# Performance work log

Hardware: AMD Instinct MI355X
Metric: run time of the kernel (lower is better)

## Reference

```python
import jax, jax.numpy as jnp
import numpy as np

NEG = -1000000.0  # mask value used by the torch module


def setup_inputs() -> dict:
    key = jax.random.key(0)
    k1, k2, k3, k4 = jax.random.split(key, 4)
    B, Q, K, D = 16, 2048, 2048, 128
    queries = jax.random.normal(k1, (B, Q, D), dtype=jnp.float32)
    keys = jax.random.normal(k2, (B, K, D), dtype=jnp.float32)
    values = jax.random.normal(k3, (B, K, D), dtype=jnp.float32)
    valid_lens = jax.random.randint(k4, (B,), 0, K, dtype=jnp.int32)
    return {"queries": queries, "keys": keys, "values": values, "valid_lens": valid_lens}


def reference(queries, keys, values, valid_lens):
    d = queries.shape[-1]
    # scores: [B, Q, K]
    scores = jnp.einsum("bqd,bkd->bqk", queries, keys) / jnp.sqrt(jnp.float32(d))
    # mask key positions >= valid_len[b] with the same -1e6 value as torch
    kv_pos = jnp.arange(scores.shape[-1])  # [K]
    mask = kv_pos[None, None, :] < valid_lens[:, None, None]  # [B,1,K]
    scores = jnp.where(mask, scores, NEG)
    attn = jax.nn.softmax(scores, axis=-1)
    # dropout p=0.0 -> identity (module in eval)
    return jnp.einsum("bqk,bkd->bqd", attn, values)
```

## Files before the change

kernel.cpp:

```cpp
#include <hip/hip_runtime.h>
#include <hip/hip_bf16.h>

#define NB    16
#define NQ    2048
#define NKV   2048
#define DH    128
#define KVT   64
#define NTILE 32
#define TILE_BYTES 16384
#define TILE_ELT   8192

typedef __attribute__((ext_vector_type(8))) short short8;
typedef __attribute__((ext_vector_type(4))) float f32x4;

__device__ __forceinline__ unsigned short f2bf(float f) {
    union { float f; unsigned int u; } x; x.f = f;
    unsigned int r = (x.u + 0x7fffu + ((x.u >> 16) & 1u)) >> 16;
    return (unsigned short)r;
}

__device__ __forceinline__ void load_lds16(const void* g, void* l) {
    __builtin_amdgcn_global_load_lds(
        (const __attribute__((address_space(1))) unsigned int*)g,
        (__attribute__((address_space(3))) unsigned int*)l, 16, 0, 0);
}

__global__ __launch_bounds__(256)
void preconv(const float* __restrict__ kg, const float* __restrict__ vg,
             const int* __restrict__ vlg,
             unsigned short* __restrict__ kws, unsigned short* __restrict__ vws) {
    __shared__ __align__(16) unsigned short lv[TILE_ELT];
    const int tid = threadIdx.x;
    const int rb = (blockIdx.x & 7) * 64 + (blockIdx.x >> 3);
    const int b = rb >> 5, t = rb & 31;
    const int vl = vlg[b];
    const int ntiles = (vl == 0) ? NTILE : ((vl + KVT - 1) >> 6);
    if (t >= ntiles) return;

    const float* kb = kg + ((size_t)b * NKV + t * KVT) * DH;
    const float* vb = vg + ((size_t)b * NKV + t * KVT) * DH;
    char* kimg = (char*)(kws + (size_t)(b * NTILE + t) * TILE_ELT);
    char* vimg = (char*)(vws + (size_t)(b * NTILE + t) * TILE_ELT);

    #pragma unroll
    for (int p = 0; p < 4; ++p) {
        int idx = p * 256 + tid;
        int row = idx >> 4, ch = idx & 15;
        f32x4 a = *(const f32x4*)(kb + row * DH + ch * 8);
        f32x4 c = *(const f32x4*)(kb + row * DH + ch * 8 + 4);
        union { short8 v; unsigned short u[8]; } w;
        #pragma unroll
        for (int j = 0; j < 4; ++j) { w.u[j] = f2bf(a[j]); w.u[4 + j] = f2bf(c[j]); }
        *(short8*)(kimg + row * 256 + ((ch * 16) ^ ((row & 7) << 4))) = w.v;
        f32x4 va = *(const f32x4*)(vb + row * DH + ch * 8);
        f32x4 vc = *(const f32x4*)(vb + row * DH + ch * 8 + 4);
        union { short8 v; unsigned short u[8]; } w2;
        #pragma unroll
        for (int j = 0; j < 4; ++j) { w2.u[j] = f2bf(va[j]); w2.u[4 + j] = f2bf(vc[j]); }
        *(short8*)((char*)lv + row * 256 + ((ch * 16) ^ (((row >> 3) & 7) << 4))) = w2.v;
    }
    __syncthreads();
    #pragma unroll
    for (int p = 0; p < 4; ++p) {
        int task = p * 256 + tid;
        int c = task & 7, d = task >> 3;
        union { short8 v; unsigned short u[8]; } w;
        #pragma unroll
        for (int j = 0; j < 8; ++j) {
            int kv = c * 8 + j;
            w.u[j] = *(const unsigned short*)((const char*)lv + kv * 256 + ((d * 2) ^ (((kv >> 3) & 7) << 4)));
        }
        *(short8*)(vimg + d * 128 + ((c * 16) ^ ((d & 7) << 4))) = w.v;
    }
}

__global__ __launch_bounds__(256, 4)
void attn_split(const float* __restrict__ qg,
                const unsigned short* __restrict__ kws,
                const unsigned short* __restrict__ vws,
                const int* __restrict__ vlg,
                float* __restrict__ og,
                float* __restrict__ opart,
                float* __restrict__ ellg,
                int S, int gmask) {
    __shared__ __align__(16) unsigned short lds_k[TILE_ELT];
    __shared__ __align__(16) unsigned short lds_v[TILE_ELT];
    __shared__ __align__(16) unsigned short lds_p[4][16 * KVT];

    const int tid = threadIdx.x;
    const int lane = tid & 63;
    const int wv = tid >> 6;
    const int row16 = lane & 15;
    const int g = lane >> 4;

    const int wid = (blockIdx.x * 1031) & gmask;
    const int b    = wid & 15;
    const int rest = wid >> 4;
    const int qt   = rest & 31;
    const int s    = rest >> 5;
    const int q0   = qt * 64 + wv * 16;
    const int vl = vlg[b];

    const int nt = (vl == 0) ? NTILE : ((vl + KVT - 1) >> 6);

    if (s >= nt) {
        if (tid < 64)
            ellg[(size_t)s * NB * NQ + (size_t)b * NQ + qt * 64 + tid] = 0.f;
        return;
    }

    const float QS = 1.4426950408889634f * 0.08838834764831845f;
    short8 qf[4];
    {
        const float* qp = qg + ((size_t)b * NQ + q0 + row16) * DH + g * 8;
        #pragma unroll
        for (int c = 0; c < 4; ++c) {
            f32x4 a  = *(const f32x4*)(qp + c * 32);
            f32x4 bb = *(const f32x4*)(qp + c * 32 + 4);
            union { short8 v; unsigned short u[8]; } t;
            #pragma unroll
            for (int j = 0; j < 4; ++j) { t.u[j] = f2bf(a[j] * QS); t.u[4 + j] = f2bf(bb[j] * QS); }
            qf[c] = t.v;
        }
    }

    const float MASKV = (vl == 0) ? 0.0f : -1442695.0f;

    f32x4 oacc[8];
    f32x4 ellacc = (f32x4){0.f, 0.f, 0.f, 0.f};
    #pragma unroll
    for (int n = 0; n < 8; ++n) oacc[n] = (f32x4){0.f, 0.f, 0.f, 0.f};
    short8 ones;
    {
        union { short8 v; unsigned short u[8]; } t;
        #pragma unroll
        for (int j = 0; j < 8; ++j) t.u[j] = 0x3F80;
        ones = t.v;
    }

    const char* kbase = (const char*)kws + (size_t)b * NTILE * TILE_BYTES;
    const char* vbase = (const char*)vws + (size_t)b * NTILE * TILE_BYTES;
    const int swzr = ((row16 >> 2) ^ ((row16 & 3) << 1)) & 7;

    for (int tt = s; tt < nt; tt += S) {
        const char* ks = kbase + (size_t)tt * TILE_BYTES;
        const char* vs = vbase + (size_t)tt * TILE_BYTES;
        #pragma unroll
        for (int i = 0; i < 4; ++i) {
            int off = i * 4096 + wv * 1024;
            load_lds16(ks + off + lane * 16, (char*)lds_k + off);
            load_lds16(vs + off + lane * 16, (char*)lds_v + off);
        }
        asm volatile("s_waitcnt vmcnt(0)" ::: "memory");
        __syncthreads();

        f32x4 sc[4];
        #pragma unroll
        for (int n = 0; n < 4; ++n) sc[n] = (f32x4){0.f, 0.f, 0.f, 0.f};
        __builtin_amdgcn_s_setprio(1);
        #pragma unroll
        for (int c = 0; c < 4; ++c) {
            short8 kf[4];
            #pragma unroll
            for (int n = 0; n < 4; ++n) {
                int krow = n * 16 + row16;
                kf[n] = *(const short8*)((const char*)lds_k + krow * 256 +
                                         ((c * 64 + g * 16) ^ ((krow & 7) << 4)));
            }
            #pragma unroll
            for (int n = 0; n < 4; ++n)
                sc[n] = __builtin_amdgcn_mfma_f32_16x16x32_bf16(qf[c], kf[n], sc[n], 0, 0, 0);
        }
        __builtin_amdgcn_s_setprio(0);

        if (vl == 0 || tt == nt - 1) {
            int kvb = tt * KVT;
            #pragma unroll
            for (int n = 0; n < 4; ++n) {
                if (kvb + n * 16 + row16 >= vl) {
                    #pragma unroll
                    for (int r = 0; r < 4; ++r) sc[n][r] = MASKV;
                }
            }
        }

        #pragma unroll
        for (int n = 0; n < 4; ++n)
            #pragma unroll
            for (int r = 0; r < 4; ++r) {
                float p = __builtin_amdgcn_exp2f(sc[n][r]);
                int qr = g * 4 + r;
                int swz = (g ^ (r << 1)) & 7;
                __hip_bfloat16 h = __float2bfloat16(p);
                *(unsigned short*)((char*)lds_p[wv] + qr * 128 +
                                   (((n * 16 + row16) * 2) ^ (swz << 4))) =
                    *reinterpret_cast<unsigned short*>(&h);
            }
        asm volatile("s_waitcnt lgkmcnt(0)" ::: "memory");

        __builtin_amdgcn_s_setprio(1);
        #pragma unroll
        for (int kc = 0; kc < 2; ++kc) {
            short8 pf = *(const short8*)((const char*)lds_p[wv] + row16 * 128 +
                                         ((kc * 64 + g * 16) ^ (swzr << 4)));
            ellacc = __builtin_amdgcn_mfma_f32_16x16x32_bf16(pf, ones, ellacc, 0, 0, 0);
            #pragma unroll
            for (int n2 = 0; n2 < 8; ++n2) {
                int vrow = n2 * 16 + row16;
                short8 vf = *(const short8*)((const char*)lds_v + vrow * 128 +
                                             ((kc * 64 + g * 16) ^ ((vrow & 7) << 4)));
                oacc[n2] = __builtin_amdgcn_mfma_f32_16x16x32_bf16(pf, vf, oacc[n2], 0, 0, 0);
            }
        }
        __builtin_amdgcn_s_setprio(0);

        __syncthreads();
    }

    if (S == 1) {
        float* ob = og + ((size_t)b * NQ + q0) * DH;
        float rl[4];
        #pragma unroll
        for (int r = 0; r < 4; ++r) rl[r] = 1.0f / ellacc[r];
        #pragma unroll
        for (int n2 = 0; n2 < 8; ++n2)
            #pragma unroll
            for (int r = 0; r < 4; ++r)
                ob[(size_t)(g * 4 + r) * DH + n2 * 16 + row16] = oacc[n2][r] * rl[r];
    } else {
        float* op = opart + ((size_t)s * NB * NQ + (size_t)b * NQ + q0) * DH;
        #pragma unroll
        for (int n2 = 0; n2 < 8; ++n2)
            #pragma unroll
            for (int r = 0; r < 4; ++r)
                op[(size_t)(g * 4 + r) * DH + n2 * 16 + row16] = oacc[n2][r];
        if (row16 == 0) {
            float* el = ellg + (size_t)s * NB * NQ + (size_t)b * NQ + q0;
            #pragma unroll
            for (int r = 0; r < 4; ++r) el[g * 4 + r] = ellacc[r];
        }
    }
}

__global__ __launch_bounds__(256)
void combine(const float* __restrict__ opart, const float* __restrict__ ellg,
             float* __restrict__ og, int S) {
    int idx = blockIdx.x * 256 + threadIdx.x;
    int row = idx >> 5;
    int c   = idx & 31;
    f32x4 acc = (f32x4){0.f, 0.f, 0.f, 0.f};
    float l = 0.f;
    for (int s = 0; s < S; ++s) {
        float le = ellg[(size_t)s * NB * NQ + row];
        if (le != 0.f) {
            acc += ((const f32x4*)opart)[((size_t)s * NB * NQ + row) * 32 + c];
            l += le;
        }
    }
    float rl = 1.0f / l;
    ((f32x4*)og)[(size_t)row * 32 + c] = acc * rl;
}

extern "C" void kernel_launch(void* const* d_in, const int* in_sizes, int n_in,
                              void* d_out, int out_size, void* d_ws, size_t ws_size,
                              hipStream_t stream) {
    const float* q  = (const float*)d_in[0];
    const float* k  = (const float*)d_in[1];
    const float* v  = (const float*)d_in[2];
    const int*   vl = (const int*)d_in[3];
    float* o = (float*)d_out;

    const size_t IMG = (size_t)NB * NTILE * TILE_BYTES;
    const size_t ELL_OFF = 2 * IMG;
    const size_t ELL_MAX = (size_t)4 * NB * NQ * 4;
    const size_t OP_OFF  = ELL_OFF + ELL_MAX;
    const size_t OP_ONE  = (size_t)NB * NQ * DH * 4;

    int S = 1;
    if (ws_size >= OP_OFF + 4 * OP_ONE) S = 4;
    else if (ws_size >= OP_OFF + 2 * OP_ONE) S = 2;

    unsigned short* kws = (unsigned short*)d_ws;
    unsigned short* vws = (unsigned short*)((char*)d_ws + IMG);
    float* ellg  = (float*)((char*)d_ws + ELL_OFF);
    float* opart = (float*)((char*)d_ws + OP_OFF);

    int grid = NB * 32 * S;
    preconv<<<dim3(NB * NTILE), dim3(256), 0, stream>>>(k, v, vl, kws, vws);
    attn_split<<<dim3(grid), dim3(256), 0, stream>>>(q, kws, vws, vl, o, opart, ellg, S, grid - 1);
    if (S > 1)
        combine<<<dim3(NB * NQ * 32 / 256), dim3(256), 0, stream>>>(opart, ellg, o, S);
}
```

Baseline: 74.66 us.

## Process 32 query rows per wave to reuse K/V LDS fragments

Each wave now handles two 16-row query blocks (128 queries per workgroup), so every K and V fragment read from LDS feeds two MFMAs, and the grid is halved. The K tile is issued before V and the kernel waits only for K before QK^T, deferring the V wait until after softmax so part of the load overlaps compute. This doubles accumulator registers and P-buffer LDS, with launch bounds lowered to 3 waves/SIMD, and halves the block count, which may hurt load balance across CUs.

```diff
diff --git a/kernel.cpp b/kernel.cpp
--- a/kernel.cpp
+++ b/kernel.cpp
@@ -74,7 +74,7 @@
     }
 }
 
-__global__ __launch_bounds__(256, 4)
+__global__ __launch_bounds__(256, 3)
 void attn_split(const float* __restrict__ qg,
                 const unsigned short* __restrict__ kws,
                 const unsigned short* __restrict__ vws,
@@ -85,7 +85,7 @@
                 int S, int gmask) {
     __shared__ __align__(16) unsigned short lds_k[TILE_ELT];
     __shared__ __align__(16) unsigned short lds_v[TILE_ELT];
-    __shared__ __align__(16) unsigned short lds_p[4][16 * KVT];
+    __shared__ __align__(16) unsigned short lds_p[4][32 * KVT];
 
     const int tid = threadIdx.x;
     const int lane = tid & 63;
@@ -94,25 +94,25 @@
     const int g = lane >> 4;
 
     const int wid = (blockIdx.x * 1031) & gmask;
-    const int b    = wid & 15;
-    const int rest = wid >> 4;
-    const int qt   = rest & 31;
-    const int s    = rest >> 5;
-    const int q0   = qt * 64 + wv * 16;
+    const int b  = wid & 15;
+    const int qt = (wid >> 4) & 15;
+    const int s  = wid >> 8;
+    const int q0 = qt * 128 + wv * 32;
     const int vl = vlg[b];
 
     const int nt = (vl == 0) ? NTILE : ((vl + KVT - 1) >> 6);
 
     if (s >= nt) {
-        if (tid < 64)
-            ellg[(size_t)s * NB * NQ + (size_t)b * NQ + qt * 64 + tid] = 0.f;
+        if (tid < 128)
+            ellg[(size_t)s * NB * NQ + (size_t)b * NQ + qt * 128 + tid] = 0.f;
         return;
     }
 
     const float QS = 1.4426950408889634f * 0.08838834764831845f;
-    short8 qf[4];
-    {
-        const float* qp = qg + ((size_t)b * NQ + q0 + row16) * DH + g * 8;
+    short8 qf[2][4];
+    #pragma unroll
+    for (int m = 0; m < 2; ++m) {
+        const float* qp = qg + ((size_t)b * NQ + q0 + m * 16 + row16) * DH + g * 8;
         #pragma unroll
         for (int c = 0; c < 4; ++c) {
             f32x4 a  = *(const f32x4*)(qp + c * 32);
@@ -120,16 +120,20 @@
             union { short8 v; unsigned short u[8]; } t;
             #pragma unroll
             for (int j = 0; j < 4; ++j) { t.u[j] = f2bf(a[j] * QS); t.u[4 + j] = f2bf(bb[j] * QS); }
-            qf[c] = t.v;
+            qf[m][c] = t.v;
         }
     }
 
     const float MASKV = (vl == 0) ? 0.0f : -1442695.0f;
 
-    f32x4 oacc[8];
-    f32x4 ellacc = (f32x4){0.f, 0.f, 0.f, 0.f};
+    f32x4 oacc[2][8];
+    f32x4 ellacc[2];
     #pragma unroll
-    for (int n = 0; n < 8; ++n) oacc[n] = (f32x4){0.f, 0.f, 0.f, 0.f};
+    for (int m = 0; m < 2; ++m) {
+        ellacc[m] = (f32x4){0.f, 0.f, 0.f, 0.f};
+        #pragma unroll
+        for (int n = 0; n < 8; ++n) oacc[m][n] = (f32x4){0.f, 0.f, 0.f, 0.f};
+    }
     short8 ones;
     {
         union { short8 v; unsigned short u[8]; } t;
@@ -149,14 +153,20 @@
         for (int i = 0; i < 4; ++i) {
             int off = i * 4096 + wv * 1024;
             load_lds16(ks + off + lane * 16, (char*)lds_k + off);
+        }
+        #pragma unroll
+        for (int i = 0; i < 4; ++i) {
+            int off = i * 4096 + wv * 1024;
             load_lds16(vs + off + lane * 16, (char*)lds_v + off);
         }
-        asm volatile("s_waitcnt vmcnt(0)" ::: "memory");
+        asm volatile("s_waitcnt vmcnt(4)" ::: "memory");
         __syncthreads();
 
-        f32x4 sc[4];
-        #pragma unroll
-        for (int n = 0; n < 4; ++n) sc[n] = (f32x4){0.f, 0.f, 0.f, 0.f};
+        f32x4 sc[2][4];
+        #pragma unroll
+        for (int m = 0; m < 2; ++m)
+            #pragma unroll
+            for (int n = 0; n < 4; ++n) sc[m][n] = (f32x4){0.f, 0.f, 0.f, 0.f};
         __builtin_amdgcn_s_setprio(1);
         #pragma unroll
         for (int c = 0; c < 4; ++c) {
@@ -169,7 +179,9 @@
             }
             #pragma unroll
             for (int n = 0; n < 4; ++n)
-                sc[n] = __builtin_amdgcn_mfma_f32_16x16x32_bf16(qf[c], kf[n], sc[n], 0, 0, 0);
+                #pragma unroll
+                for (int m = 0; m < 2; ++m)
+                    sc[m][n] = __builtin_amdgcn_mfma_f32_16x16x32_bf16(qf[m][c], kf[n], sc[m][n], 0, 0, 0);
         }
         __builtin_amdgcn_s_setprio(0);
 
@@ -179,37 +191,50 @@
             for (int n = 0; n < 4; ++n) {
                 if (kvb + n * 16 + row16 >= vl) {
                     #pragma unroll
-                    for (int r = 0; r < 4; ++r) sc[n][r] = MASKV;
+                    for (int m = 0; m < 2; ++m)
+                        #pragma unroll
+                        for (int r = 0; r < 4; ++r) sc[m][n][r] = MASKV;
                 }
             }
         }
 
         #pragma unroll
-        for (int n = 0; n < 4; ++n)
-            #pragma unroll
-            for (int r = 0; r < 4; ++r) {
-                float p = __builtin_amdgcn_exp2f(sc[n][r]);
-                int qr = g * 4 + r;
-                int swz = (g ^ (r << 1)) & 7;
-                __hip_bfloat16 h = __float2bfloat16(p);
-                *(unsigned short*)((char*)lds_p[wv] + qr * 128 +
-                                   (((n * 16 + row16) * 2) ^ (swz << 4))) =
-                    *reinterpret_cast<unsigned short*>(&h);
+        for (int m = 0; m < 2; ++m)
+            #pragma unroll
+            for (int n = 0; n < 4; ++n)
+                #pragma unroll
+                for (int r = 0; r < 4; ++r) {
+                    float p = __builtin_amdgcn_exp2f(sc[m][n][r]);
+                    int qr = m * 16 + g * 4 + r;
+                    int swz = (g ^ (r << 1)) & 7;
+                    __hip_bfloat16 h = __float2bfloat16(p);
+                    *(unsigned short*)((char*)lds_p[wv] + qr * 128 +
+                                       (((n * 16 + row16) * 2) ^ (swz << 4))) =
+                        *reinterpret_cast<unsigned short*>(&h);
+                }
+        asm volatile("s_waitcnt lgkmcnt(0)" ::: "memory");
+
+        asm volatile("s_waitcnt vmcnt(0)" ::: "memory");
+        __syncthreads();
+
+        __builtin_amdgcn_s_setprio(1);
+        #pragma unroll
+        for (int kc = 0; kc < 2; ++kc) {
+            short8 pf[2];
+            #pragma unroll
+            for (int m = 0; m < 2; ++m) {
+                pf[m] = *(const short8*)((const char*)lds_p[wv] + (m * 16 + row16) * 128 +
+                                         ((kc * 64 + g * 16) ^ (swzr << 4)));
+                ellacc[m] = __builtin_amdgcn_mfma_f32_16x16x32_bf16(pf[m], ones, ellacc[m], 0, 0, 0);
             }
-        asm volatile("s_waitcnt lgkmcnt(0)" ::: "memory");
-
-        __builtin_amdgcn_s_setprio(1);
-        #pragma unroll
-        for (int kc = 0; kc < 2; ++kc) {
-            short8 pf = *(const short8*)((const char*)lds_p[wv] + row16 * 128 +
-                                         ((kc * 64 + g * 16) ^ (swzr << 4)));
-            ellacc = __builtin_amdgcn_mfma_f32_16x16x32_bf16(pf, ones, ellacc, 0, 0, 0);
             #pragma unroll
             for (int n2 = 0; n2 < 8; ++n2) {
                 int vrow = n2 * 16 + row16;
                 short8 vf = *(const short8*)((const char*)lds_v + vrow * 128 +
                                              ((kc * 64 + g * 16) ^ ((vrow & 7) << 4)));
-                oacc[n2] = __builtin_amdgcn_mfma_f32_16x16x32_bf16(pf, vf, oacc[n2], 0, 0, 0);
+                #pragma unroll
+                for (int m = 0; m < 2; ++m)
+                    oacc[m][n2] = __builtin_amdgcn_mfma_f32_16x16x32_bf16(pf[m], vf, oacc[m][n2], 0, 0, 0);
             }
         }
         __builtin_amdgcn_s_setprio(0);
@@ -219,25 +244,32 @@
 
     if (S == 1) {
         float* ob = og + ((size_t)b * NQ + q0) * DH;
-        float rl[4];
-        #pragma unroll
-        for (int r = 0; r < 4; ++r) rl[r] = 1.0f / ellacc[r];
-        #pragma unroll
-        for (int n2 = 0; n2 < 8; ++n2)
-            #pragma unroll
-            for (int r = 0; r < 4; ++r)
-                ob[(size_t)(g * 4 + r) * DH + n2 * 16 + row16] = oacc[n2][r] * rl[r];
+        #pragma unroll
+        for (int m = 0; m < 2; ++m) {
+            float rl[4];
+            #pragma unroll
+            for (int r = 0; r < 4; ++r) rl[r] = 1.0f / ellacc[m][r];
+            #pragma unroll
+            for (int n2 = 0; n2 < 8; ++n2)
+                #pragma unroll
+                for (int r = 0; r < 4; ++r)
+                    ob[(size_t)(m * 16 + g * 4 + r) * DH + n2 * 16 + row16] = oacc[m][n2][r] * rl[r];
+        }
     } else {
         float* op = opart + ((size_t)s * NB * NQ + (size_t)b * NQ + q0) * DH;
         #pragma unroll
-        for (int n2 = 0; n2 < 8; ++n2)
-            #pragma unroll
-            for (int r = 0; r < 4; ++r)
-                op[(size_t)(g * 4 + r) * DH + n2 * 16 + row16] = oacc[n2][r];
+        for (int m = 0; m < 2; ++m)
+            #pragma unroll
+            for (int n2 = 0; n2 < 8; ++n2)
+                #pragma unroll
+                for (int r = 0; r < 4; ++r)
+                    op[(size_t)(m * 16 + g * 4 + r) * DH + n2 * 16 + row16] = oacc[m][n2][r];
         if (row16 == 0) {
             float* el = ellg + (size_t)s * NB * NQ + (size_t)b * NQ + q0;
             #pragma unroll
-            for (int r = 0; r < 4; ++r) el[g * 4 + r] = ellacc[r];
+            for (int m = 0; m < 2; ++m)
+                #pragma unroll
+                for (int r = 0; r < 4; ++r) el[m * 16 + g * 4 + r] = ellacc[m][r];
         }
     }
 }
@@ -285,7 +317,7 @@
     float* ellg  = (float*)((char*)d_ws + ELL_OFF);
     float* opart = (float*)((char*)d_ws + OP_OFF);
 
-    int grid = NB * 32 * S;
+    int grid = NB * 16 * S;
     preconv<<<dim3(NB * NTILE), dim3(256), 0, stream>>>(k, v, vl, kws, vws);
     attn_split<<<dim3(grid), dim3(256), 0, stream>>>(q, kws, vws, vl, o, opart, ellg, S, grid - 1);
     if (S > 1)
```

After: 85.01 us. 1.14x slower.
